# Optimization experiments

Measured on AMD Instinct MI355X. Metric: run time of the kernel, lower is better.

The kernel has to match this reference:

```python
import jax, jax.numpy as jnp
import numpy as np

H = 16          # num_heads
NB = 32         # pos_bias_num_buckets
EPS = 1e-8      # RMSNorm eps


def setup_inputs() -> dict:
    key = jax.random.key(0)
    ks = jax.random.split(key, 8)
    B, L, K, R, M, Dm, Dq = 2, 32, 2, 64, 128, 2048, 2048
    x = jax.random.normal(ks[0], (B, L, K, R, Dm), jnp.float32)
    past_ca_hidden_states = jax.random.normal(ks[1], (B, L, M, Dm), jnp.float32)
    past_ca_attention_mask = jax.random.bernoulli(ks[2], 0.95, (B, L, M)).astype(jnp.float32)
    ln_scale = jnp.ones((Dm,), jnp.float32)
    q_w = jax.random.normal(ks[3], (Dq, Dm), jnp.float32) * 0.02      # torch Linear weight [out,in]
    kv_w = jax.random.normal(ks[4], (2 * Dq, Dm), jnp.float32) * 0.02
    out_w = jax.random.normal(ks[5], (Dm, Dq), jnp.float32) * 0.02
    bias_table = jax.random.normal(ks[6], (NB, H), jnp.float32) * 0.02  # relative_attention_bias.weight
    return dict(x=x, past_ca_hidden_states=past_ca_hidden_states,
                past_ca_attention_mask=past_ca_attention_mask,
                ln_scale=ln_scale, q_w=q_w, kv_w=kv_w, out_w=out_w,
                bias_table=bias_table)


def _rel_bias(bias_table, r, m):
    # linear bucketing, bidirectional=True (RelativePositionBias._relative_position_bucket_linear)
    mn = -(NB // 2) - (NB % 2 - 1)   # -15 for NB=32
    mx = NB // 2                      # 16
    rel = jnp.arange(m)[None, :] - jnp.arange(r)[:, None]   # memory - query, [r, m]
    buckets = jnp.clip(rel, mn, mx) - mn                    # in [0, NB)
    return jnp.transpose(bias_table[buckets], (2, 0, 1))    # [H, r, m]


def reference(x, past_ca_hidden_states, past_ca_attention_mask,
              ln_scale, q_w, kv_w, out_w, bias_table):
    B, L, K, R, Dm = x.shape
    M = past_ca_hidden_states.shape[2]
    Dq = q_w.shape[0]
    dh = Dq // H

    # RMSNorm (p=-1: full norm)
    rms = jnp.linalg.norm(x, axis=-1, keepdims=True) * (Dm ** -0.5)
    xn = (x / (rms + EPS)) * ln_scale

    # projections (no bias)
    q = jnp.einsum('blkrc,qc->blkrq', xn, q_w)                 # [B,L,K,R,Dq]
    kv = jnp.einsum('blmc,qc->blmq', past_ca_hidden_states, kv_w)  # [B,L,M,2Dq]
    k = kv[..., :Dq]
    v = kv[..., Dq:]

    # split heads
    q = q.reshape(B, L, K, R, H, dh).transpose(0, 1, 2, 4, 3, 5)  # [B,L,K,H,R,dh]
    k = k.reshape(B, L, M, H, dh).transpose(0, 1, 3, 2, 4)        # [B,L,H,M,dh]
    v = v.reshape(B, L, M, H, dh).transpose(0, 1, 3, 2, 4)        # [B,L,H,M,dh]

    # NOTE: original applies NO 1/sqrt(dh) scaling
    scores = jnp.einsum('blkhrd,blhmd->blkhrm', q, k)             # [B,L,K,H,R,M]
    scores = scores + _rel_bias(bias_table, R, M)                 # broadcast [H,R,M]
    mask_add = (1.0 - past_ca_attention_mask) * -10000.0          # [B,L,M]
    scores = scores + mask_add[:, :, None, None, None, :]

    attn = jax.nn.softmax(scores, axis=-1)
    out = jnp.einsum('blkhrm,blhmd->blkhrd', attn, v)             # [B,L,K,H,R,dh]
    out = out.transpose(0, 1, 2, 4, 3, 5).reshape(B, L, K, R, Dq)  # merge heads '(h d)'
    out = jnp.einsum('blkrq,cq->blkrc', out, out_w)                # final_proj
    return out + x, attn
```

## Files before the change

kernel.cpp:

```cpp
#include <hip/hip_runtime.h>

typedef _Float16 f16;
typedef _Float16 f16x8 __attribute__((ext_vector_type(8)));
typedef float f32x4 __attribute__((ext_vector_type(4)));

#define LDS_GL16(g, l) __builtin_amdgcn_global_load_lds( \
    (const __attribute__((address_space(1))) void*)(g),  \
    (__attribute__((address_space(3))) void*)(l), 16, 0, 0)
#define VMCNT(N) asm volatile("s_waitcnt vmcnt(" #N ")" ::: "memory")
#define BAR() __builtin_amdgcn_s_barrier()

__global__ __launch_bounds__(256) void conv_kern(const float* __restrict__ in,
                                                 f16* __restrict__ out, int n8) {
    int i = blockIdx.x * 256 + threadIdx.x;
    if (i >= n8) return;
    long o = (long)i * 8;
    float4 a = *(const float4*)(in + o);
    float4 b = *(const float4*)(in + o + 4);
    f16x8 v = { (f16)a.x,(f16)a.y,(f16)a.z,(f16)a.w,
                (f16)b.x,(f16)b.y,(f16)b.z,(f16)b.w };
    *(f16x8*)(out + o) = v;
}

__global__ __launch_bounds__(256) void rmsnorm_kern(const float* __restrict__ x,
                                                    const float* __restrict__ scale,
                                                    f16* __restrict__ out) {
    long base = (long)blockIdx.x * 2048 + threadIdx.x * 8;
    float4 a = *(const float4*)(x + base);
    float4 b = *(const float4*)(x + base + 4);
    float ss = a.x*a.x + a.y*a.y + a.z*a.z + a.w*a.w
             + b.x*b.x + b.y*b.y + b.z*b.z + b.w*b.w;
    #pragma unroll
    for (int d = 1; d < 64; d <<= 1) ss += __shfl_xor(ss, d, 64);
    __shared__ float red[4];
    if ((threadIdx.x & 63) == 0) red[threadIdx.x >> 6] = ss;
    __syncthreads();
    ss = red[0] + red[1] + red[2] + red[3];
    float inv = 1.0f / (sqrtf(ss * (1.0f / 2048.0f)) + 1e-8f);
    int c = threadIdx.x * 8;
    float4 s1 = *(const float4*)(scale + c);
    float4 s2 = *(const float4*)(scale + c + 4);
    f16x8 v = { (f16)(a.x*inv*s1.x),(f16)(a.y*inv*s1.y),(f16)(a.z*inv*s1.z),(f16)(a.w*inv*s1.w),
                (f16)(b.x*inv*s2.x),(f16)(b.y*inv*s2.y),(f16)(b.z*inv*s2.z),(f16)(b.w*inv*s2.w) };
    *(f16x8*)(out + base) = v;
}

template<int EPI>
__global__ __launch_bounds__(512, 2) void gemm256(
        const f16* __restrict__ A, const f16* __restrict__ B,
        f16* __restrict__ Ch, float* __restrict__ Cf,
        const float* __restrict__ resid, int M, int N, int Kd) {
    alignas(16) __shared__ f16 lds[65536];
    int nbx = N >> 8;
    int cpx = gridDim.x >> 3;
    int fid = (blockIdx.x & 7) * cpx + (blockIdx.x >> 3);
    int by = fid / nbx, bx = fid % nbx;
    int m0 = by << 8, n0 = bx << 8;
    int tid = threadIdx.x, lane = tid & 63;
    int wid = tid >> 6, wm = wid >> 2, wn = wid & 3;
    int lr = lane & 15, g = lane >> 4;
    int iL = tid >> 3, cb = tid & 7;

    auto stage = [&](int kt, int p, int r) {
        #pragma unroll
        for (int rnd = 0; rnd < 2; ++rnd) {
            if (r == 0 || r == 3) {
                int row = iL + rnd * 128 + (r == 3 ? 64 : 0);
                LDS_GL16(A + (long)(m0 + row) * Kd + kt * 64 + ((cb ^ (row & 7)) << 3),
                         lds + p * 16384 + row * 64 + (cb << 3));
            } else {
                int row = (iL & 31) + ((iL >> 5) + rnd * 2) * 64 + (r == 2 ? 32 : 0);
                LDS_GL16(B + (long)(n0 + row) * Kd + kt * 64 + ((cb ^ (row & 7)) << 3),
                         lds + 32768 + p * 16384 + row * 64 + (cb << 3));
            }
        }
    };

    f32x4 acc[8][4] = {};
    f16x8 a[4][2], b0[2][2], b1[2][2];

    auto loadA = [&](const f16* bp, int qm) {
        #pragma unroll
        for (int mf = 0; mf < 4; ++mf) {
            int row = wm * 128 + (qm * 4 + mf) * 16 + lr;
            #pragma unroll
            for (int kk = 0; kk < 2; ++kk)
                a[mf][kk] = *(const f16x8*)(bp + row * 64 + (((kk * 4 + g) ^ (row & 7)) << 3));
        }
    };
    auto loadB = [&](f16x8 (&d)[2][2], const f16* bp, int qn) {
        #pragma unroll
        for (int nf = 0; nf < 2; ++nf) {
            int row = wn * 64 + (qn * 2 + nf) * 16 + lr;
            #pragma unroll
            for (int kk = 0; kk < 2; ++kk)
                d[nf][kk] = *(const f16x8*)(bp + row * 64 + (((kk * 4 + g) ^ (row & 7)) << 3));
        }
    };
    auto mma = [&](f16x8 (&bb)[2][2], int qm, int qn) {
        __builtin_amdgcn_s_setprio(1);
        #pragma unroll
        for (int mf = 0; mf < 4; ++mf)
            #pragma unroll
            for (int nf = 0; nf < 2; ++nf)
                #pragma unroll
                for (int kk = 0; kk < 2; ++kk)
                    acc[qm * 4 + mf][qn * 2 + nf] = __builtin_amdgcn_mfma_f32_16x16x32_f16(
                        a[mf][kk], bb[nf][kk], acc[qm * 4 + mf][qn * 2 + nf], 0, 0, 0);
        __builtin_amdgcn_s_setprio(0);
    };

    const f16* A0p = lds;
    const f16* A1p = lds + 16384;
    const f16* B0p = lds + 32768;
    const f16* B1p = lds + 49152;
    int NT = Kd >> 6, NI = NT >> 1;

    stage(0, 0, 0); stage(0, 0, 1); stage(0, 0, 2); stage(0, 0, 3);
    stage(1, 1, 0); stage(1, 1, 1); stage(1, 1, 2);
    VMCNT(6); BAR();

    for (int it = 0; it < NI - 1; ++it) {
        int t0 = it * 2;
        loadA(A0p, 0); loadB(b0, B0p, 0);
        stage(t0 + 1, 1, 3);
        VMCNT(6); BAR(); mma(b0, 0, 0); BAR();
        loadB(b1, B0p, 1);
        stage(t0 + 2, 0, 0);
        VMCNT(6); BAR(); mma(b1, 0, 1); BAR();
        loadA(A0p, 1);
        stage(t0 + 2, 0, 1);
        VMCNT(6); BAR(); mma(b1, 1, 1); BAR();
        stage(t0 + 2, 0, 2);
        VMCNT(6); BAR(); mma(b0, 1, 0); BAR();
        loadA(A1p, 0); loadB(b0, B1p, 0);
        stage(t0 + 2, 0, 3);
        VMCNT(6); BAR(); mma(b0, 0, 0); BAR();
        loadB(b1, B1p, 1);
        stage(t0 + 3, 1, 0);
        VMCNT(6); BAR(); mma(b1, 0, 1); BAR();
        loadA(A1p, 1);
        stage(t0 + 3, 1, 1);
        VMCNT(6); BAR(); mma(b1, 1, 1); BAR();
        stage(t0 + 3, 1, 2);
        VMCNT(6); BAR(); mma(b0, 1, 0); BAR();
    }
    {
        loadA(A0p, 0); loadB(b0, B0p, 0);
        stage(NT - 1, 1, 3);
        VMCNT(6); BAR(); mma(b0, 0, 0); BAR();
        loadB(b1, B0p, 1);
        VMCNT(6); BAR(); mma(b1, 0, 1); BAR();
        loadA(A0p, 1);
        VMCNT(6); BAR(); mma(b1, 1, 1); BAR();
        VMCNT(4); BAR(); mma(b0, 1, 0); BAR();
        loadA(A1p, 0); loadB(b0, B1p, 0);
        VMCNT(2); BAR(); mma(b0, 0, 0); BAR();
        loadB(b1, B1p, 1);
        VMCNT(0); BAR(); mma(b1, 0, 1); BAR();
        loadA(A1p, 1);
        BAR(); mma(b1, 1, 1); BAR();
        BAR(); mma(b0, 1, 0); BAR();
    }

    #pragma unroll
    for (int i = 0; i < 8; ++i) {
        #pragma unroll
        for (int j = 0; j < 4; ++j) {
            #pragma unroll
            for (int reg = 0; reg < 4; ++reg) {
                int row = m0 + wm * 128 + i * 16 + g * 4 + reg;
                int col = n0 + wn * 64 + j * 16 + lr;
                long idx = (long)row * N + col;
                float v = acc[i][j][reg];
                if (EPI == 0) Ch[idx] = (f16)v;
                else          Cf[idx] = v + resid[idx];
            }
        }
    }
}

__global__ __launch_bounds__(256, 2) void attn_kern(
        const f16* __restrict__ Q,
        const f16* __restrict__ KV,
        const float* __restrict__ mask,
        const float* __restrict__ bias,
        float* __restrict__ attn_out,
        f16* __restrict__ pv_out) {
    __shared__ f16 Vs[128 * 128];
    __shared__ f16 P[64 * 136];
    int blk = blockIdx.x;
    int h  = blk & 15;
    int bk = blk >> 4;
    int bl = bk >> 1;
    int tid = threadIdx.x, lane = tid & 63, w = tid >> 6;
    int r0 = w << 4;
    int lr = lane & 15, g = lane >> 4;
    long qbase  = (long)bk * 64 * 2048;
    long kvbase = (long)bl * 128 * 4096;
    const f16* vsrc = KV + kvbase + 2048 + h * 128;
    {
        int idx = tid;
        #pragma unroll
        for (int rnd = 0; rnd < 8; ++rnd) {
            int vrow = idx >> 4, c = idx & 15;
            LDS_GL16(vsrc + (long)vrow * 4096 + c * 8, Vs + idx * 8);
            idx += 256;
        }
    }
    f16x8 aq[4];
    const f16* qrow = Q + qbase + (long)(r0 + lr) * 2048 + h * 128 + g * 8;
    #pragma unroll
    for (int t4 = 0; t4 < 4; ++t4) aq[t4] = *(const f16x8*)(qrow + t4 * 32);
    f32x4 s[8] = {};
    const f16* kbase = KV + kvbase + h * 128 + g * 8;
    #pragma unroll
    for (int j = 0; j < 8; ++j) {
        #pragma unroll
        for (int t4 = 0; t4 < 4; ++t4) {
            f16x8 bkf = *(const f16x8*)(kbase + (long)(j * 16 + lr) * 4096 + t4 * 32);
            s[j] = __builtin_amdgcn_mfma_f32_16x16x32_f16(aq[t4], bkf, s[j], 0, 0, 0);
        }
    }
    float madd[8];
    #pragma unroll
    for (int j = 0; j < 8; ++j)
        madd[j] = (1.0f - mask[(long)bl * 128 + j * 16 + lr]) * -10000.0f;
    #pragma unroll
    for (int reg = 0; reg < 4; ++reg) {
        int r = r0 + g * 4 + reg;
        float mx = -3.0e38f;
        #pragma unroll
        for (int j = 0; j < 8; ++j) {
            int m = j * 16 + lr;
            int rel = m - r;
            int bkt = (rel < -15 ? -15 : (rel > 16 ? 16 : rel)) + 15;
            float v = s[j][reg] + bias[bkt * 16 + h] + madd[j];
            s[j][reg] = v;
            mx = fmaxf(mx, v);
        }
        #pragma unroll
        for (int d = 1; d < 16; d <<= 1) mx = fmaxf(mx, __shfl_xor(mx, d, 64));
        float sum = 0.0f;
        #pragma unroll
        for (int j = 0; j < 8; ++j) {
            float e = __expf(s[j][reg] - mx);
            s[j][reg] = e;
            sum += e;
        }
        #pragma unroll
        for (int d = 1; d < 16; d <<= 1) sum += __shfl_xor(sum, d, 64);
        float inv = 1.0f / sum;
        #pragma unroll
        for (int j = 0; j < 8; ++j) s[j][reg] *= inv;
    }
    long abase = (long)blk * 64 * 128;
    #pragma unroll
    for (int reg = 0; reg < 4; ++reg) {
        int r = r0 + g * 4 + reg;
        #pragma unroll
        for (int j = 0; j < 8; ++j) {
            attn_out[abase + (long)r * 128 + j * 16 + lr] = s[j][reg];
            P[r * 136 + j * 16 + lr] = (f16)s[j][reg];
        }
    }
    __syncthreads();
    f16x8 pa[4];
    #pragma unroll
    for (int t4 = 0; t4 < 4; ++t4)
        pa[t4] = *(const f16x8*)(P + (r0 + lr) * 136 + t4 * 32 + g * 8);
    f32x4 o[8] = {};
    #pragma unroll
    for (int dj = 0; dj < 8; ++dj) {
        #pragma unroll
        for (int t4 = 0; t4 < 4; ++t4) {
            f16x8 bv;
            #pragma unroll
            for (int rg = 0; rg < 8; ++rg)
                bv[rg] = Vs[(t4 * 32 + g * 8 + rg) * 128 + dj * 16 + lr];
            o[dj] = __builtin_amdgcn_mfma_f32_16x16x32_f16(pa[t4], bv, o[dj], 0, 0, 0);
        }
    }
    f16* ob = pv_out + qbase + h * 128;
    #pragma unroll
    for (int dj = 0; dj < 8; ++dj)
        #pragma unroll
        for (int reg = 0; reg < 4; ++reg)
            ob[(long)(r0 + g * 4 + reg) * 2048 + dj * 16 + lr] = (f16)o[dj][reg];
}

extern "C" void kernel_launch(void* const* d_in, const int* in_sizes, int n_in,
                              void* d_out, int out_size, void* d_ws, size_t ws_size,
                              hipStream_t stream) {
    const float* x     = (const float*)d_in[0];
    const float* hid   = (const float*)d_in[1];
    const float* mask  = (const float*)d_in[2];
    const float* lnsc  = (const float*)d_in[3];
    const float* q_w   = (const float*)d_in[4];
    const float* kv_w  = (const float*)d_in[5];
    const float* out_w = (const float*)d_in[6];
    const float* bias  = (const float*)d_in[7];
    float* out0 = (float*)d_out;
    float* attn = out0 + 16777216;

    f16* kv_h  = (f16*)out0;
    f16* xn_h  = (f16*)attn;
    f16* hid_h = (f16*)(attn + 8388608);
    char* ws = (char*)d_ws;
    f16* q_h    = (f16*)(ws);
    f16* ao_h   = (f16*)(ws + 33554432L);
    f16* qw_h   = (f16*)(ws + 67108864L);
    f16* kvw_h  = (f16*)(ws + 75497472L);
    f16* outw_h = (f16*)(ws + 92274688L);

    conv_kern<<<2048, 256, 0, stream>>>(q_w,   qw_h,   524288);
    conv_kern<<<4096, 256, 0, stream>>>(kv_w,  kvw_h, 1048576);
    conv_kern<<<2048, 256, 0, stream>>>(out_w, outw_h, 524288);
    conv_kern<<<8192, 256, 0, stream>>>(hid,   hid_h, 2097152);
    rmsnorm_kern<<<8192, 256, 0, stream>>>(x, lnsc, xn_h);
    gemm256<0><<<256, 512, 0, stream>>>(xn_h, qw_h, q_h, nullptr, nullptr,
                                        8192, 2048, 2048);
    gemm256<0><<<512, 512, 0, stream>>>(hid_h, kvw_h, kv_h, nullptr, nullptr,
                                        8192, 4096, 2048);
    attn_kern<<<2048, 256, 0, stream>>>(q_h, kv_h, mask, bias, attn, ao_h);
    gemm256<1><<<256, 512, 0, stream>>>(ao_h, outw_h, nullptr, out0, x,
                                        8192, 2048, 2048);
}
```

Before: 403.7 us.

## Merge fp32-to-fp16 conversions into one launch and relax GEMM vmcnt waits

The four separate conversion kernels become one kernel that picks its source and destination buffer from the block index, which removes three launches. In the GEMM main loop the vmcnt wait now runs only once per half-iteration instead of before every MMA step, so more global-to-LDS loads can be in flight. This relies on the stage/buffer scheduling guaranteeing that data is ready when consumed. Any mistake in that reasoning becomes a race, and the final trailing barrier was also removed.

```diff
diff --git a/kernel.cpp b/kernel.cpp
--- a/kernel.cpp
+++ b/kernel.cpp
@@ -10,15 +10,22 @@
 #define VMCNT(N) asm volatile("s_waitcnt vmcnt(" #N ")" ::: "memory")
 #define BAR() __builtin_amdgcn_s_barrier()
 
-__global__ __launch_bounds__(256) void conv_kern(const float* __restrict__ in,
-                                                 f16* __restrict__ out, int n8) {
-    int i = blockIdx.x * 256 + threadIdx.x;
-    if (i >= n8) return;
-    long o = (long)i * 8;
+__global__ __launch_bounds__(256) void conv4_kern(
+        const float* __restrict__ s0, f16* __restrict__ d0,
+        const float* __restrict__ s1, f16* __restrict__ d1,
+        const float* __restrict__ s2, f16* __restrict__ d2,
+        const float* __restrict__ s3, f16* __restrict__ d3) {
+    int b = blockIdx.x;
+    const float* in; f16* out; long base;
+    if (b < 2048)       { in = s0; out = d0; base = (long)b * 2048; }
+    else if (b < 6144)  { in = s1; out = d1; base = (long)(b - 2048) * 2048; }
+    else if (b < 8192)  { in = s2; out = d2; base = (long)(b - 6144) * 2048; }
+    else                { in = s3; out = d3; base = (long)(b - 8192) * 2048; }
+    long o = base + threadIdx.x * 8;
     float4 a = *(const float4*)(in + o);
-    float4 b = *(const float4*)(in + o + 4);
+    float4 c = *(const float4*)(in + o + 4);
     f16x8 v = { (f16)a.x,(f16)a.y,(f16)a.z,(f16)a.w,
-                (f16)b.x,(f16)b.y,(f16)b.z,(f16)b.w };
+                (f16)c.x,(f16)c.y,(f16)c.z,(f16)c.w };
     *(f16x8*)(out + o) = v;
 }
 
@@ -124,43 +131,46 @@
         int t0 = it * 2;
         loadA(A0p, 0); loadB(b0, B0p, 0);
         stage(t0 + 1, 1, 3);
-        VMCNT(6); BAR(); mma(b0, 0, 0); BAR();
+        BAR(); mma(b0, 0, 0); BAR();
         loadB(b1, B0p, 1);
         stage(t0 + 2, 0, 0);
-        VMCNT(6); BAR(); mma(b1, 0, 1); BAR();
+        BAR(); mma(b1, 0, 1); BAR();
         loadA(A0p, 1);
         stage(t0 + 2, 0, 1);
-        VMCNT(6); BAR(); mma(b1, 1, 1); BAR();
+        BAR(); mma(b1, 1, 1); BAR();
         stage(t0 + 2, 0, 2);
-        VMCNT(6); BAR(); mma(b0, 1, 0); BAR();
+        VMCNT(6);
+        BAR(); mma(b0, 1, 0); BAR();
         loadA(A1p, 0); loadB(b0, B1p, 0);
         stage(t0 + 2, 0, 3);
-        VMCNT(6); BAR(); mma(b0, 0, 0); BAR();
+        BAR(); mma(b0, 0, 0); BAR();
         loadB(b1, B1p, 1);
         stage(t0 + 3, 1, 0);
-        VMCNT(6); BAR(); mma(b1, 0, 1); BAR();
+        BAR(); mma(b1, 0, 1); BAR();
         loadA(A1p, 1);
         stage(t0 + 3, 1, 1);
-        VMCNT(6); BAR(); mma(b1, 1, 1); BAR();
+        BAR(); mma(b1, 1, 1); BAR();
         stage(t0 + 3, 1, 2);
-        VMCNT(6); BAR(); mma(b0, 1, 0); BAR();
+        VMCNT(6);
+        BAR(); mma(b0, 1, 0); BAR();
     }
     {
         loadA(A0p, 0); loadB(b0, B0p, 0);
         stage(NT - 1, 1, 3);
-        VMCNT(6); BAR(); mma(b0, 0, 0); BAR();
+        BAR(); mma(b0, 0, 0); BAR();
         loadB(b1, B0p, 1);
-        VMCNT(6); BAR(); mma(b1, 0, 1); BAR();
+        BAR(); mma(b1, 0, 1); BAR();
         loadA(A0p, 1);
-        VMCNT(6); BAR(); mma(b1, 1, 1); BAR();
-        VMCNT(4); BAR(); mma(b0, 1, 0); BAR();
+        BAR(); mma(b1, 1, 1); BAR();
+        VMCNT(0);
+        BAR(); mma(b0, 1, 0); BAR();
         loadA(A1p, 0); loadB(b0, B1p, 0);
-        VMCNT(2); BAR(); mma(b0, 0, 0); BAR();
+        BAR(); mma(b0, 0, 0); BAR();
         loadB(b1, B1p, 1);
-        VMCNT(0); BAR(); mma(b1, 0, 1); BAR();
+        BAR(); mma(b1, 0, 1); BAR();
         loadA(A1p, 1);
         BAR(); mma(b1, 1, 1); BAR();
-        BAR(); mma(b0, 1, 0); BAR();
+        BAR(); mma(b0, 1, 0);
     }
 
     #pragma unroll
@@ -313,10 +323,8 @@
     f16* kvw_h  = (f16*)(ws + 75497472L);
     f16* outw_h = (f16*)(ws + 92274688L);
 
-    conv_kern<<<2048, 256, 0, stream>>>(q_w,   qw_h,   524288);
-    conv_kern<<<4096, 256, 0, stream>>>(kv_w,  kvw_h, 1048576);
-    conv_kern<<<2048, 256, 0, stream>>>(out_w, outw_h, 524288);
-    conv_kern<<<8192, 256, 0, stream>>>(hid,   hid_h, 2097152);
+    conv4_kern<<<16384, 256, 0, stream>>>(q_w, qw_h, kv_w, kvw_h,
+                                          out_w, outw_h, hid, hid_h);
     rmsnorm_kern<<<8192, 256, 0, stream>>>(x, lnsc, xn_h);
     gemm256<0><<<256, 512, 0, stream>>>(xn_h, qw_h, q_h, nullptr, nullptr,
                                         8192, 2048, 2048);
```

Result: no change. 397.0 us (-1.7%).
